# Kernel tuning notes

Measured on AMD Instinct MI355X. Metric: run time of the kernel, lower is better.

## Reference

```python
import jax, jax.numpy as jnp
import numpy as np

NUM_SAMPLES = 512
FG_FRACTION = 0.25
MAX_POS = int(NUM_SAMPLES * FG_FRACTION)  # 128
THRESHOLDS = np.array([0.0, 0.5, 0.5], dtype=np.float32)
INDICATORS = np.array([-3, -1, -2, 1], dtype=np.int32)


def _make_boxes(key, shape, scale):
    # random valid boxes: sorted corner pairs in [0, scale)
    y = jnp.sort(jax.random.uniform(key, shape[:-1] + (2,)) * scale, axis=-1)
    x = jnp.sort(jax.random.uniform(jax.random.fold_in(key, 1), shape[:-1] + (2,)) * scale, axis=-1)
    return jnp.stack([y[..., 0], x[..., 0], y[..., 1], x[..., 1]], axis=-1)


def setup_inputs() -> dict:
    key = jax.random.key(0)
    k1, k2, k3, k4 = jax.random.split(key, 4)
    B, N, M = 32, 8000, 256
    boxes = _make_boxes(k1, (B, N, 4), 1024.0)
    gt_boxes = _make_boxes(k2, (B, M, 4), 1024.0)
    # pad last quarter of gt entries with -1 (invalid)
    valid = (jnp.arange(M) < (3 * M) // 4)[None, :, None]
    gt_boxes = jnp.where(valid, gt_boxes, -jnp.ones_like(gt_boxes))
    gt_classes = jax.random.randint(k3, (B, M), 1, 91, dtype=jnp.int32)
    gt_classes = jnp.where(valid[..., 0], gt_classes, -1)
    rand = jax.random.uniform(k4, (B, N + M))
    return {"boxes": boxes, "gt_boxes": gt_boxes, "gt_classes": gt_classes, "rand": rand}


def _pairwise_iou(b1, b2):
    # b1: [B,N,4], b2: [B,M,4] in (ymin,xmin,ymax,xmax) -> [B,N,M]
    ymin1, xmin1, ymax1, xmax1 = jnp.split(b1, 4, axis=-1)  # each [B,N,1]
    ymin2, xmin2, ymax2, xmax2 = (t[..., 0] for t in jnp.split(b2, 4, axis=-1))  # [B,M]
    ih = jnp.clip(jnp.minimum(ymax1, ymax2[:, None, :]) - jnp.maximum(ymin1, ymin2[:, None, :]), 0.0)
    iw = jnp.clip(jnp.minimum(xmax1, xmax2[:, None, :]) - jnp.maximum(xmin1, xmin2[:, None, :]), 0.0)
    inter = ih * iw
    a1 = (ymax1 - ymin1) * (xmax1 - xmin1)          # [B,N,1]
    a2 = (ymax2 - ymin2) * (xmax2 - xmin2)          # [B,M]
    union = a1 + a2[:, None, :] - inter
    return jnp.where(union > 0, inter / union, 0.0)


def _ranks_desc(score):
    order = jnp.argsort(-score)
    return jnp.zeros_like(order).at[order].set(jnp.arange(score.shape[0]))


def _sample_one(pos, neg, ign, rand):
    cand = (pos | neg) & ~ign
    pos_c = pos & cand
    neg_c = neg & cand
    pos_rank = _ranks_desc(jnp.where(pos_c, rand, -1.0))
    pos_sel = pos_c & (pos_rank < MAX_POS)
    neg_needed = NUM_SAMPLES - jnp.sum(pos_sel)
    neg_rank = _ranks_desc(jnp.where(neg_c, rand, -1.0))
    neg_sel = neg_c & (neg_rank < neg_needed)
    indicator = (pos_sel | neg_sel).astype(jnp.int32)
    _, idx = jax.lax.top_k(indicator, NUM_SAMPLES)  # selected first, ties by lowest index
    return idx


def _gather(t, idx):
    # t: [B,L,C], idx: [B,K] -> [B,K,C]
    return jnp.take_along_axis(t, idx[..., None], axis=1)


def reference(boxes, gt_boxes, gt_classes, rand):
    gt_boxes = gt_boxes.astype(boxes.dtype)
    boxes = jnp.concatenate([boxes, gt_boxes], axis=1)  # mix_gt_boxes
    boxes_invalid = jnp.max(boxes, axis=-1) < 0.0       # [B,L]
    gt_invalid = jnp.max(gt_boxes, axis=-1) < 0.0       # [B,M]
    sim = _pairwise_iou(boxes, gt_boxes)                # [B,L,M]
    sim = jnp.where(boxes_invalid[:, :, None] | gt_invalid[:, None, :], -1.0, sim)

    matched_vals = jnp.max(sim, axis=-1)                # [B,L]
    matched_gt_indices = jnp.argmax(sim, axis=-1).astype(jnp.int32)
    bucket = jnp.searchsorted(jnp.asarray(THRESHOLDS), matched_vals, side='right')
    match_indicators = jnp.asarray(INDICATORS)[bucket]  # [B,L]

    positive = match_indicators >= 0
    negative = match_indicators == -1
    ignored = match_indicators == -2
    invalid = match_indicators == -3
    background = negative | invalid                     # [B,L]

    matched_gt_classes = _gather(gt_classes[..., None], matched_gt_indices)[..., 0]
    matched_gt_classes = jnp.where(background, 0, matched_gt_classes)
    matched_gt_boxes = _gather(gt_boxes, matched_gt_indices)
    matched_gt_boxes = jnp.where(background[..., None], 0.0, matched_gt_boxes)
    matched_gt_indices = jnp.where(background, -1, matched_gt_indices)

    indices = jax.vmap(_sample_one)(positive, negative, ignored, rand)  # [B,K]
    rois = _gather(boxes, indices)
    sampled_gt_boxes = _gather(matched_gt_boxes, indices)
    sampled_gt_classes = _gather(matched_gt_classes[..., None], indices)[..., 0]
    sampled_gt_indices = _gather(matched_gt_indices[..., None], indices)[..., 0]
    return rois, sampled_gt_boxes, sampled_gt_classes, sampled_gt_indices
```

## Files before the change

### kernel.cpp

```cpp
#include <hip/hip_runtime.h>
#include <stdint.h>

#define BB 32
#define NN 8000
#define MM 256
#define LL (NN + MM)
#define NSAMP 512
#define MAXPOS 128
#define T2 1024
#define CH ((LL + T2 - 1) / T2)
#define SPLIT 4
#define MSUB (MM / SPLIT)
#define ONE_P 1.0000019073486328f
#define ONE_M 0.9999980926513672f

__device__ __forceinline__ void opaquef(float& x) { asm("" : "+v"(x)); }

__device__ __noinline__ void serial_argmax_q(const float4 bx, const float a1,
                                             const float4* s_gt, const float* s_a2,
                                             int* obi, float* oq)
{
    float qb = -1.0f; int bi = 0;
    for (int m = 0; m < MSUB; ++m) {
        float4 g = s_gt[m];
        float ih = fmaxf(fminf(bx.z, g.z) - fmaxf(bx.x, g.x), 0.0f);
        float iw = fmaxf(fminf(bx.w, g.w) - fmaxf(bx.y, g.y), 0.0f);
        float inter = ih * iw; opaquef(inter);
        float uni = (a1 + s_a2[m]) - inter;
        float q = (uni > 0.0f) ? (inter / uni) : 0.0f;
        if (q > qb) { qb = q; bi = m; }
    }
    *obi = bi; *oq = qb;
}

__global__ __launch_bounds__(256) void match_split_kernel(
    const float* __restrict__ boxes, const float* __restrict__ gt,
    unsigned long long* __restrict__ keymax)
{
    __shared__ float4 s_gt[MSUB];
    __shared__ float  s_a2[MSUB];
    const int b = blockIdx.y, sp = blockIdx.z, tid = threadIdx.x;
    if (tid < MSUB) {
        float4 v = ((const float4*)(gt + ((size_t)b * MM + sp * MSUB) * 4))[tid];
        s_gt[tid] = v;
        s_a2[tid] = (v.z - v.x) * (v.w - v.y);
    }
    __syncthreads();
    const int l0 = blockIdx.x * 512 + tid * 2;
    if (l0 >= LL) return;
    const int l1 = l0 + 1;
    const bool v1 = (l1 < LL);
    const int l1c = v1 ? l1 : l0;

    const float4* bb4 = (const float4*)(boxes + (size_t)b * NN * 4);
    const float4* gb4 = (const float4*)(gt + (size_t)b * MM * 4);
    float4 bx0 = (l0 < NN) ? bb4[l0] : gb4[l0 - NN];
    float4 bx1 = (l1c < NN) ? bb4[l1c] : gb4[l1c - NN];
    float a10 = (bx0.z - bx0.x) * (bx0.w - bx0.y); opaquef(a10);
    float a11 = (bx1.z - bx1.x) * (bx1.w - bx1.y); opaquef(a11);
    const bool binv0 = fmaxf(fmaxf(bx0.x, bx0.y), fmaxf(bx0.z, bx0.w)) < 0.0f;
    const bool binv1 = fmaxf(fmaxf(bx1.x, bx1.y), fmaxf(bx1.z, bx1.w)) < 0.0f;

    float I00 = 0.f, S00 = 1.f, I01 = 0.f, S01 = 1.f;
    float I10 = 0.f, S10 = 1.f, I11 = 0.f, S11 = 1.f;
    int X00 = 0, X01 = 1, X10 = 0, X11 = 1;
    bool redo0 = false, redo1 = false;

    #define STEP(BX, A1, G, A2, BI, BS, BIX, MIDX, RD)                       \
    {                                                                        \
        float ih = fmaxf(fminf(BX.z, G.z) - fmaxf(BX.x, G.x), 0.0f);         \
        float iw = fmaxf(fminf(BX.w, G.w) - fmaxf(BX.y, G.y), 0.0f);         \
        float inter = ih * iw; opaquef(inter);                               \
        float s  = A1 + A2;                                                  \
        float p1 = inter * BS, p2 = BI * s;                                  \
        bool win = p1 > p2 * ONE_P;                                          \
        RD |= ((p1 > p2 * ONE_M) != win);                                    \
        if (win) { BI = inter; BS = s; BIX = MIDX; }                         \
    }
    #pragma unroll 4
    for (int m = 0; m < MSUB; m += 2) {
        float4 g0 = s_gt[m];     float a2_0 = s_a2[m];
        float4 g1 = s_gt[m + 1]; float a2_1 = s_a2[m + 1];
        STEP(bx0, a10, g0, a2_0, I00, S00, X00, m,     redo0)
        STEP(bx0, a10, g1, a2_1, I01, S01, X01, m + 1, redo0)
        STEP(bx1, a11, g0, a2_0, I10, S10, X10, m,     redo1)
        STEP(bx1, a11, g1, a2_1, I11, S11, X11, m + 1, redo1)
    }
    #undef STEP

    #define MERGE(I0, S0, X0, I1, S1, X1, RD)                                \
    {                                                                        \
        float p1 = I1 * S0, p2 = I0 * S1;                                    \
        bool win = p1 > p2 * ONE_P;                                          \
        RD |= ((p1 > p2 * ONE_M) != win);                                    \
        if (win) { I0 = I1; S0 = S1; X0 = X1; }                              \
    }
    MERGE(I00, S00, X00, I01, S01, X01, redo0)
    MERGE(I10, S10, X10, I11, S11, X11, redo1)
    #undef MERGE

    float q0, q1; int m0 = X00, m1 = X10;
    if (__any(redo0 || redo1)) {
        if (redo0) serial_argmax_q(bx0, a10, s_gt, s_a2, &m0, &q0);
        if (redo1) serial_argmax_q(bx1, a11, s_gt, s_a2, &m1, &q1);
    }
    if (!redo0) {
        float uni = S00 - I00;
        q0 = (uni > 0.0f) ? (I00 / uni) : 0.0f;
    }
    if (!redo1) {
        float uni = S10 - I10;
        q1 = (uni > 0.0f) ? (I10 / uni) : 0.0f;
    }
    if (!binv0) {
        unsigned long long key =
            (((unsigned long long)(__float_as_uint(q0) + 1u)) << 32)
            | (unsigned long long)(255 - (sp * MSUB + m0));
        atomicMax(&keymax[(size_t)b * LL + l0], key);
    }
    if (v1 && !binv1) {
        unsigned long long key =
            (((unsigned long long)(__float_as_uint(q1) + 1u)) << 32)
            | (unsigned long long)(255 - (sp * MSUB + m1));
        atomicMax(&keymax[(size_t)b * LL + l1], key);
    }
}

__device__ __forceinline__ int block_exscan_fast(int v, int* wt, int tid)
{
    const int lane = tid & 63, w = tid >> 6;
    int x = v;
    #pragma unroll
    for (int off = 1; off < 64; off <<= 1) {
        int y = __shfl_up(x, off);
        if (lane >= off) x += y;
    }
    if (lane == 63) wt[w] = x;
    __syncthreads();
    if (tid < 64) {
        int t = (tid < 16) ? wt[tid] : 0;
        #pragma unroll
        for (int off = 1; off < 16; off <<= 1) {
            int y = __shfl_up(t, off);
            if (tid >= off) t += y;
        }
        if (tid < 16) wt[tid] = t;
    }
    __syncthreads();
    return ((w > 0) ? wt[w - 1] : 0) + x - v;
}

__device__ __forceinline__ int block_exscan_seg4(int v, int* wt, int tid)
{
    const int lane = tid & 63, w = tid >> 6;
    int x = v;
    #pragma unroll
    for (int off = 1; off < 64; off <<= 1) {
        int y = __shfl_up(x, off);
        if (lane >= off) x += y;
    }
    if (lane == 63) wt[w] = x;
    __syncthreads();
    if (tid < 16) {
        int t = wt[tid];
        #pragma unroll
        for (int off = 1; off < 4; off <<= 1) {
            int y = __shfl_up(t, off);
            if ((tid & 3) >= off) t += y;
        }
        wt[tid] = t;
    }
    __syncthreads();
    return (((w & 3) > 0) ? wt[w - 1] : 0) + x - v;
}

__global__ __launch_bounds__(T2) void sample_kernel(
    const float* __restrict__ boxes, const float* __restrict__ gt,
    const int* __restrict__ gtc, const float* __restrict__ rnd,
    const unsigned long long* __restrict__ keymax, float* __restrict__ out)
{
    __shared__ uint32_t s_key[LL];
    __shared__ uint16_t s_pk[LL];
    __shared__ int s_hist[512];
    __shared__ int s_warp[16];
    __shared__ int s_idx[NSAMP];
    __shared__ int s_sb[8];
    const int b = blockIdx.x, tid = threadIdx.x, lane = tid & 63;
    const float4* bb4 = (const float4*)(boxes + (size_t)b * NN * 4);
    const float4* gb4 = (const float4*)(gt + (size_t)b * MM * 4);

    if (tid == 0) s_sb[0] = 0;
    __syncthreads();

    int loc = 0;
    for (int l = tid; l < LL; l += T2) {
        s_key[l] = __float_as_uint(rnd[(size_t)b * LL + l]);
        const unsigned long long kk = keymax[(size_t)b * LL + l];
        uint16_t p;
        if (kk == 0ull) {
            p = 2;
        } else {
            const uint32_t qb = (uint32_t)(kk >> 32) - 1u;
            const int gidx = 255 - (int)(kk & 0xFFull);
            const int cls = (qb >= 0x3F000000u) ? 1 : 0;
            p = (uint16_t)(cls | (gidx << 2));
        }
        s_pk[l] = p;
        int c = p & 3;
        loc += (c == 0) ? 1 : ((c == 1) ? 0x10000 : 0);
    }
    #pragma unroll
    for (int off = 32; off; off >>= 1) loc += __shfl_xor(loc, off);
    if (lane == 0) atomicAdd(&s_sb[0], loc);
    __syncthreads();
    const int Nn = s_sb[0] & 0xFFFF, P = s_sb[0] >> 16;

    const int posK = (P < MAXPOS) ? P : MAXPOS;
    const int negK = NSAMP - posK;
    const bool negRad = (Nn > negK);
    const bool posRad = (P > MAXPOS);

    uint32_t prefix0 = 0, prefix1 = 0;
    int rem0 = negK, rem1 = MAXPOS;
    bool act0 = negRad, act1 = posRad;
    uint32_t thr0f = 0, thr1f = 0;
    int r0f = LL, r1f = LL;
    for (int round = 0; round < 4 && (act0 || act1); ++round) {
        const int shift = 24 - 8 * round;
        if (tid < 512) s_hist[tid] = 0;
        __syncthreads();
        const uint32_t pmask = (round == 0) ? 0u : (0xFFFFFFFFu << (shift + 8));
        for (int l = tid; l < LL; l += T2) {
            const uint32_t k = s_key[l];
            const int c = s_pk[l] & 3;
            bool doit = (c == 0) ? (act0 && ((k & pmask) == prefix0))
                      : (c == 1) ? (act1 && ((k & pmask) == prefix1))
                      : false;
            if (doit) atomicAdd(&s_hist[(c << 8) | ((k >> shift) & 255)], 1);
        }
        __syncthreads();
        int h = 0;
        if (tid < 512) h = s_hist[(tid & 0x100) | (255 - (tid & 255))];
        const int above = block_exscan_seg4(h, s_warp, tid);
        if (tid < 512) {
            const int c = tid >> 8;
            const int rem = c ? rem1 : rem0;
            const bool act = c ? act1 : act0;
            if (act && above < rem && above + h >= rem) {
                s_sb[4 + c * 2] = 255 - (tid & 255);
                s_sb[5 + c * 2] = above;
            }
        }
        __syncthreads();
        if (act0) {
            const int bin = s_sb[4];
            rem0 -= s_sb[5];
            prefix0 |= ((uint32_t)bin) << shift;
            const int cnt = s_hist[bin];
            if (rem0 == cnt)      { act0 = false; thr0f = prefix0; r0f = LL; }
            else if (round == 3)  { act0 = false; thr0f = prefix0; r0f = rem0; }
        }
        if (act1) {
            const int bin = s_sb[6];
            rem1 -= s_sb[7];
            prefix1 |= ((uint32_t)bin) << shift;
            const int cnt = s_hist[256 + bin];
            if (rem1 == cnt)      { act1 = false; thr1f = prefix1; r1f = LL; }
            else if (round == 3)  { act1 = false; thr1f = prefix1; r1f = rem1; }
        }
        __syncthreads();
    }
    const uint32_t thr0 = negRad ? thr0f : 0u;  const int r0 = negRad ? r0f : LL;
    const uint32_t thr1 = posRad ? thr1f : 0u;  const int r1 = posRad ? r1f : LL;

    const int lo = tid * CH, hi = (lo + CH < LL) ? (lo + CH) : LL;
    int nt = 0;
    for (int l = lo; l < hi; ++l) {
        const int c = s_pk[l] & 3;
        const uint32_t k = s_key[l];
        if (c == 0) { if (k == thr0) nt += 1; }
        else if (c == 1) { if (k == thr1) nt += 0x10000; }
    }
    const int basep = block_exscan_fast(nt, s_warp, tid);
    int base0 = basep & 0xFFFF, base1 = basep >> 16;
    for (int l = lo; l < hi; ++l) {
        const int c = s_pk[l] & 3;
        if (c > 1) continue;
        const uint32_t k = s_key[l];
        const uint32_t thr = c ? thr1 : thr0;
        bool sel = (k > thr);
        if (k == thr) {
            if (c == 0) { sel = (base0 < r0); ++base0; }
            else        { sel = (base1 < r1); ++base1; }
        }
        if (sel) s_pk[l] |= 0x8000;
    }
    __syncthreads();

    int cnt = 0;
    for (int l = lo; l < hi; ++l) cnt += (s_pk[l] & 0x8000) ? 1 : 0x10000;
    const int pb = block_exscan_fast(cnt, s_warp, tid);
    const int S = s_warp[15] & 0xFFFF;
    int bs = pb & 0xFFFF, bu = (pb >> 16) + S;
    for (int l = lo; l < hi; ++l) {
        if (s_pk[l] & 0x8000) { if (bs < NSAMP) s_idx[bs] = l; ++bs; }
        else                  { if (bu < NSAMP) s_idx[bu] = l; ++bu; }
    }
    __syncthreads();

    if (tid < NSAMP) {
        const int l = s_idx[tid];
        float4 bx = (l < NN) ? bb4[l] : gb4[l - NN];
        const int p = s_pk[l];
        const int c = p & 3, mi = (p >> 2) & 0xFF;
        const bool bg = (c != 1);
        float4 gb = make_float4(0.f, 0.f, 0.f, 0.f);
        int cl = 0, si = -1;
        if (!bg) {
            gb = gb4[mi];
            cl = gtc[(size_t)b * MM + mi];
            si = mi;
        }
        const size_t rk = (size_t)b * NSAMP + tid;
        ((float4*)out)[rk] = bx;
        ((float4*)(out + (size_t)BB * NSAMP * 4))[rk] = gb;
        out[(size_t)2 * BB * NSAMP * 4 + rk] = (float)cl;
        out[(size_t)2 * BB * NSAMP * 4 + (size_t)BB * NSAMP + rk] = (float)si;
    }
}

extern "C" void kernel_launch(void* const* d_in, const int* in_sizes, int n_in,
                              void* d_out, int out_size, void* d_ws, size_t ws_size,
                              hipStream_t stream)
{
    const float* boxes = (const float*)d_in[0];
    const float* gt    = (const float*)d_in[1];
    const int*   gtc   = (const int*)  d_in[2];
    const float* rnd   = (const float*)d_in[3];
    float* out = (float*)d_out;
    unsigned long long* keymax = (unsigned long long*)d_ws;

    hipMemsetAsync(d_ws, 0, (size_t)BB * LL * 8, stream);
    dim3 g1((LL + 511) / 512, BB, SPLIT);
    match_split_kernel<<<g1, 256, 0, stream>>>(boxes, gt, keymax);
    sample_kernel<<<BB, T2, 0, stream>>>(boxes, gt, gtc, rnd, keymax, out);
}
```

Baseline: 73.02 us.

## Replace global 64-bit atomicMax merge with per-split 32-bit keys reduced in sampler

Each split block now writes a packed 32-bit key (truncated IoU bits plus local index) into its own slot instead of doing a 64-bit atomicMax into a shared array. This removes the memset launch and the atomics. The sample kernel reads all four split keys as one uint4 and picks the maximum. When truncated keys tie across splits, it recomputes exact IoU for the tied candidates. This adds a small recompute path and the cost of reading four keys per element.

```diff
diff --git a/kernel.cpp b/kernel.cpp
--- a/kernel.cpp
+++ b/kernel.cpp
@@ -35,7 +35,7 @@
 
 __global__ __launch_bounds__(256) void match_split_kernel(
     const float* __restrict__ boxes, const float* __restrict__ gt,
-    unsigned long long* __restrict__ keymax)
+    uint32_t* __restrict__ keys)
 {
     __shared__ float4 s_gt[MSUB];
     __shared__ float  s_a2[MSUB];
@@ -112,17 +112,13 @@
         float uni = S10 - I10;
         q1 = (uni > 0.0f) ? (I10 / uni) : 0.0f;
     }
-    if (!binv0) {
-        unsigned long long key =
-            (((unsigned long long)(__float_as_uint(q0) + 1u)) << 32)
-            | (unsigned long long)(255 - (sp * MSUB + m0));
-        atomicMax(&keymax[(size_t)b * LL + l0], key);
-    }
-    if (v1 && !binv1) {
-        unsigned long long key =
-            (((unsigned long long)(__float_as_uint(q1) + 1u)) << 32)
-            | (unsigned long long)(255 - (sp * MSUB + m1));
-        atomicMax(&keymax[(size_t)b * LL + l1], key);
+    uint32_t k0 = binv0 ? 0u
+        : ((__float_as_uint(q0) & 0xFFFFFFC0u) | (uint32_t)(63 - m0));
+    keys[((size_t)b * LL + l0) * SPLIT + sp] = k0;
+    if (v1) {
+        uint32_t k1 = binv1 ? 0u
+            : ((__float_as_uint(q1) & 0xFFFFFFC0u) | (uint32_t)(63 - m1));
+        keys[((size_t)b * LL + l1) * SPLIT + sp] = k1;
     }
 }
 
@@ -177,7 +173,7 @@
 __global__ __launch_bounds__(T2) void sample_kernel(
     const float* __restrict__ boxes, const float* __restrict__ gt,
     const int* __restrict__ gtc, const float* __restrict__ rnd,
-    const unsigned long long* __restrict__ keymax, float* __restrict__ out)
+    const uint32_t* __restrict__ keys, float* __restrict__ out)
 {
     __shared__ uint32_t s_key[LL];
     __shared__ uint16_t s_pk[LL];
@@ -195,15 +191,47 @@
     int loc = 0;
     for (int l = tid; l < LL; l += T2) {
         s_key[l] = __float_as_uint(rnd[(size_t)b * LL + l]);
-        const unsigned long long kk = keymax[(size_t)b * LL + l];
+        const uint4 kv = ((const uint4*)keys)[(size_t)b * LL + l];
+        uint32_t best = kv.x; int bsp = 0;
+        if (kv.y > best) { best = kv.y; bsp = 1; }
+        if (kv.z > best) { best = kv.z; bsp = 2; }
+        if (kv.w > best) { best = kv.w; bsp = 3; }
         uint16_t p;
-        if (kk == 0ull) {
+        if (best == 0u) {
             p = 2;
         } else {
-            const uint32_t qb = (uint32_t)(kk >> 32) - 1u;
-            const int gidx = 255 - (int)(kk & 0xFFull);
-            const int cls = (qb >= 0x3F000000u) ? 1 : 0;
-            p = (uint16_t)(cls | (gidx << 2));
+            const uint32_t bt = best & ~63u;
+            const uint32_t e0 = (bsp == 0) ? 0u : (kv.x & ~63u);
+            const uint32_t e1 = (bsp == 1) ? 0u : (kv.y & ~63u);
+            const uint32_t e2 = (bsp == 2) ? 0u : (kv.z & ~63u);
+            const uint32_t e3 = (bsp == 3) ? 0u : (kv.w & ~63u);
+            const uint32_t sec = max(max(e0, e1), max(e2, e3));
+            int cls, midx;
+            if (bt > sec) {
+                midx = bsp * MSUB + (63 - (int)(best & 63u));
+                cls = (bt >= 0x3F000000u) ? 1 : 0;
+            } else {
+                float4 bx = (l < NN) ? bb4[l] : gb4[l - NN];
+                float a1 = (bx.z - bx.x) * (bx.w - bx.y); opaquef(a1);
+                float qb = -1.0f; midx = 0;
+                #pragma unroll
+                for (int sp = 0; sp < SPLIT; ++sp) {
+                    const uint32_t k = (sp == 0) ? kv.x : (sp == 1) ? kv.y
+                                     : (sp == 2) ? kv.z : kv.w;
+                    if (k == 0u) continue;
+                    const int m = sp * MSUB + (63 - (int)(k & 63u));
+                    float4 g = gb4[m];
+                    float a2 = (g.z - g.x) * (g.w - g.y); opaquef(a2);
+                    float ih = fmaxf(fminf(bx.z, g.z) - fmaxf(bx.x, g.x), 0.0f);
+                    float iw = fmaxf(fminf(bx.w, g.w) - fmaxf(bx.y, g.y), 0.0f);
+                    float inter = ih * iw; opaquef(inter);
+                    float uni = (a1 + a2) - inter;
+                    float q = (uni > 0.0f) ? (inter / uni) : 0.0f;
+                    if (q > qb) { qb = q; midx = m; }
+                }
+                cls = (qb >= 0.5f) ? 1 : 0;
+            }
+            p = (uint16_t)(cls | (midx << 2));
         }
         s_pk[l] = p;
         int c = p & 3;
@@ -338,10 +366,9 @@
     const int*   gtc   = (const int*)  d_in[2];
     const float* rnd   = (const float*)d_in[3];
     float* out = (float*)d_out;
-    unsigned long long* keymax = (unsigned long long*)d_ws;
-
-    hipMemsetAsync(d_ws, 0, (size_t)BB * LL * 8, stream);
+    uint32_t* keys = (uint32_t*)d_ws;
+
     dim3 g1((LL + 511) / 512, BB, SPLIT);
-    match_split_kernel<<<g1, 256, 0, stream>>>(boxes, gt, keymax);
-    sample_kernel<<<BB, T2, 0, stream>>>(boxes, gt, gtc, rnd, keymax, out);
-}
+    match_split_kernel<<<g1, 256, 0, stream>>>(boxes, gt, keys);
+    sample_kernel<<<BB, T2, 0, stream>>>(boxes, gt, gtc, rnd, keys, out);
+}
```

Result: faster. 71.58 us (-2.0%).
